# Performance work log

Measured on AMD Instinct MI355X. Metric: run time of the kernel, lower is better.

The kernel has to match this reference:

```python
import jax, jax.numpy as jnp
import numpy as np

B, L, DIM, H = 1, 2048, 3072, 24
D = DIM // H  # 128
EPS = 1e-6

def setup_inputs() -> dict:
    key = jax.random.key(0)
    ks = jax.random.split(key, 7)
    x = jax.random.normal(ks[0], (B, L, DIM), dtype=jnp.float32)
    pe = jax.random.normal(ks[1], (B, 1, L, D // 2, 2, 2), dtype=jnp.float32)
    w_qkv = jax.random.normal(ks[2], (DIM, 3 * DIM), dtype=jnp.float32) / np.sqrt(DIM)
    q_scale = jnp.ones((D,), dtype=jnp.float32)
    k_scale = jnp.ones((D,), dtype=jnp.float32)
    w_proj = jax.random.normal(ks[3], (DIM, DIM), dtype=jnp.float32) / np.sqrt(DIM)
    b_proj = jnp.zeros((DIM,), dtype=jnp.float32)
    return {"x": x, "pe": pe, "w_qkv": w_qkv, "q_scale": q_scale,
            "k_scale": k_scale, "w_proj": w_proj, "b_proj": b_proj}

def _rmsnorm(t, scale):
    # flax nn.RMSNorm: t * rsqrt(mean(t^2, -1) + eps) * scale
    ms = jnp.mean(jnp.square(t), axis=-1, keepdims=True)
    return t * jax.lax.rsqrt(ms + EPS) * scale

def _apply_rope(xq, xk, pe):
    # xq/xk: [B,H,L,D]; pe: [B,1,L,D/2,2,2]
    xq_ = xq.reshape(*xq.shape[:-1], -1, 1, 2)
    xk_ = xk.reshape(*xk.shape[:-1], -1, 1, 2)
    xq_out = pe[..., 0] * xq_[..., 0] + pe[..., 1] * xq_[..., 1]
    xk_out = pe[..., 0] * xk_[..., 0] + pe[..., 1] * xk_[..., 1]
    return xq_out.reshape(xq.shape), xk_out.reshape(xk.shape)

def reference(x, pe, w_qkv, q_scale, k_scale, w_proj, b_proj):
    qkv = jnp.einsum('bld,de->ble', x, w_qkv)            # [B,L,3*DIM]
    qkv = qkv.reshape(B, L, 3, H, D)
    qkv = jnp.moveaxis(qkv, 2, 0)                          # [3,B,H?,..]
    q, k, v = jnp.transpose(qkv, (0, 1, 3, 2, 4))          # each [B,H,L,D]
    q = _rmsnorm(q, q_scale).astype(v.dtype)
    k = _rmsnorm(k, k_scale).astype(v.dtype)
    q, k = _apply_rope(q, k, pe)
    scale = 1.0 / np.sqrt(D)
    scores = jnp.einsum('bhqd,bhkd->bhqk', q, k) * scale   # [B,H,L,L]
    attn = jax.nn.softmax(scores, axis=-1)
    out = jnp.einsum('bhqk,bhkd->bhqd', attn, v)           # [B,H,L,D]
    out = jnp.transpose(out, (0, 2, 1, 3)).reshape(B, L, DIM)
    return jnp.einsum('bld,de->ble', out, w_proj) + b_proj
```

## Files before the change

### kernel.cpp

```cpp
#include <hip/hip_runtime.h>

#define L_    2048
#define DIM_  3072
#define H_    24
#define D_    128
#define NQKV  9216

typedef __attribute__((ext_vector_type(8))) short bf16x8;
typedef __attribute__((ext_vector_type(4))) short bf16x4;
typedef __attribute__((ext_vector_type(4))) float f32x4;

__device__ __forceinline__ unsigned short f2bf(float f) {
  union { float f; unsigned u; } v; v.f = f;
  unsigned r = v.u + 0x7fffu + ((v.u >> 16) & 1u);
  return (unsigned short)(r >> 16);
}
__device__ __forceinline__ float bf2f(unsigned short h) {
  union { unsigned u; float f; } v; v.u = ((unsigned)h) << 16;
  return v.f;
}

__device__ __forceinline__ void gload_lds16(const void* g, void* l) {
  auto* lp = reinterpret_cast<__attribute__((address_space(3))) unsigned int*>(
      reinterpret_cast<uintptr_t>(l));
  auto* gp = reinterpret_cast<const __attribute__((address_space(1))) unsigned int*>(
      reinterpret_cast<uintptr_t>(g));
  __builtin_amdgcn_global_load_lds(gp, lp, 16, 0, 0);
}

__global__ void cast_f32_to_bf16(const float* __restrict__ in,
                                 unsigned short* __restrict__ out, int n) {
  int total = n >> 2;
  int stride = gridDim.x * blockDim.x;
  for (int i = blockIdx.x * blockDim.x + threadIdx.x; i < total; i += stride) {
    float4 v = ((const float4*)in)[i];
    ushort4 o;
    o.x = f2bf(v.x); o.y = f2bf(v.y); o.z = f2bf(v.z); o.w = f2bf(v.w);
    ((ushort4*)out)[i] = o;
  }
}

__global__ __launch_bounds__(256)
void castT_f32_bf16(const float* __restrict__ in, unsigned short* __restrict__ out,
                    int K, int N) {
  int k = blockIdx.x * 256 + threadIdx.x;
  int n0 = blockIdx.y * 128;
  const float* src = in + (size_t)k * N;
  #pragma unroll 8
  for (int j = 0; j < 128; j++)
    out[(size_t)(n0 + j) * K + k] = f2bf(src[n0 + j]);
}

template<bool OUT_BF16, bool BIAS>
__global__ __launch_bounds__(256, 3)
void gemm_bt(const unsigned short* __restrict__ A,
             const unsigned short* __restrict__ Bt,
             void* __restrict__ Cout, const float* __restrict__ bias,
             int M, int N, int K)
{
  __shared__ unsigned short As[128 * 64];
  __shared__ unsigned short Bs[128 * 64];
  const int tid  = threadIdx.x;
  const int wave = tid >> 6;
  const int lane = tid & 63;
  const int l15  = lane & 15;
  const int quad = lane >> 4;
  const int wm = wave >> 1, wn = wave & 1;
  const int bm = blockIdx.y * 128;
  const int bn = blockIdx.x * 128;

  const int srow = lane >> 3;
  const int scol = (lane & 7) ^ srow;
  const unsigned short* Ag = A  + (size_t)(bm + wave * 32 + srow) * K + scol * 8;
  const unsigned short* Bg = Bt + (size_t)(bn + wave * 32 + srow) * K + scol * 8;
  unsigned short* Al = &As[(wave * 32) * 64];
  unsigned short* Bl = &Bs[(wave * 32) * 64];

  f32x4 acc[4][4];
  #pragma unroll
  for (int i = 0; i < 4; i++)
    #pragma unroll
    for (int j = 0; j < 4; j++) acc[i][j] = (f32x4){0.f, 0.f, 0.f, 0.f};

  for (int k0 = 0; k0 < K; k0 += 64) {
    __syncthreads();
    #pragma unroll
    for (int j = 0; j < 4; j++) {
      gload_lds16(Ag + (size_t)j * 8 * K + k0, Al + j * 8 * 64);
      gload_lds16(Bg + (size_t)j * 8 * K + k0, Bl + j * 8 * 64);
    }
    __syncthreads();
    #pragma unroll
    for (int ks = 0; ks < 2; ks++) {
      const int cph = ((ks * 4 + quad) ^ (l15 & 7)) * 8;
      bf16x8 af[4], bf[4];
      #pragma unroll
      for (int mt = 0; mt < 4; mt++)
        af[mt] = *(const bf16x8*)&As[(wm * 64 + mt * 16 + l15) * 64 + cph];
      #pragma unroll
      for (int nt = 0; nt < 4; nt++)
        bf[nt] = *(const bf16x8*)&Bs[(wn * 64 + nt * 16 + l15) * 64 + cph];
      #pragma unroll
      for (int mt = 0; mt < 4; mt++)
        #pragma unroll
        for (int nt = 0; nt < 4; nt++)
          acc[mt][nt] = __builtin_amdgcn_mfma_f32_16x16x32_bf16(
              af[mt], bf[nt], acc[mt][nt], 0, 0, 0);
    }
  }
  #pragma unroll
  for (int mt = 0; mt < 4; mt++)
    #pragma unroll
    for (int nt = 0; nt < 4; nt++)
      #pragma unroll
      for (int r = 0; r < 4; r++) {
        int row = bm + wm * 64 + mt * 16 + quad * 4 + r;
        int col = bn + wn * 64 + nt * 16 + l15;
        float v = acc[mt][nt][r];
        if (BIAS) v += bias[col];
        if (OUT_BF16)
          ((unsigned short*)Cout)[(size_t)row * N + col] = f2bf(v);
        else
          ((float*)Cout)[(size_t)row * N + col] = v;
      }
}

__global__ __launch_bounds__(128)
void qkv_post(const unsigned short* __restrict__ qkv,
              const float* __restrict__ pe,
              const float* __restrict__ q_scale,
              const float* __restrict__ k_scale,
              unsigned short* __restrict__ Qo,
              unsigned short* __restrict__ Ko)
{
  const int l = blockIdx.x;
  const int h = blockIdx.y;
  const int d = threadIdx.x;
  const int wave = d >> 6;
  const unsigned short* row = qkv + (size_t)l * NQKV + h * D_;
  float qv = bf2f(row[d]);
  float kv = bf2f(row[DIM_ + d]);
  float q2 = qv * qv, k2 = kv * kv;
  #pragma unroll
  for (int mask = 1; mask < 64; mask <<= 1) {
    q2 += __shfl_xor(q2, mask);
    k2 += __shfl_xor(k2, mask);
  }
  __shared__ float sq[2], sk[2];
  __shared__ float qbuf[128], kbuf[128];
  if ((d & 63) == 0) { sq[wave] = q2; sk[wave] = k2; }
  __syncthreads();
  float msq = (sq[0] + sq[1]) * (1.f / 128.f);
  float msk = (sk[0] + sk[1]) * (1.f / 128.f);
  qbuf[d] = qv * rsqrtf(msq + 1e-6f) * q_scale[d];
  kbuf[d] = kv * rsqrtf(msk + 1e-6f) * k_scale[d];
  __syncthreads();
  int p = d >> 1, s = d & 1;
  const float* pel = pe + (((size_t)l * 64 + p) * 2 + s) * 2;
  float a = pel[0], b = pel[1];
  float qr = (a * qbuf[2 * p] + b * qbuf[2 * p + 1]) * 0.08838834764831845f;
  float kr =  a * kbuf[2 * p] + b * kbuf[2 * p + 1];
  size_t o = ((size_t)h * L_ + l) * D_ + d;
  Qo[o] = f2bf(qr);
  Ko[o] = f2bf(kr);
}

__global__ __launch_bounds__(256)
void v_transpose(const unsigned short* __restrict__ qkv,
                 unsigned short* __restrict__ Vt) {
  int h = blockIdx.y;
  int l = blockIdx.x * 256 + threadIdx.x;
  const unsigned short* src = qkv + (size_t)l * NQKV + 2 * DIM_ + h * D_;
  unsigned short* dst = Vt + (size_t)h * D_ * L_ + l;
  #pragma unroll
  for (int c = 0; c < 16; c++) {
    uint4 v = *(const uint4*)&src[c * 8];
    const unsigned short* pv = (const unsigned short*)&v;
    #pragma unroll
    for (int j = 0; j < 8; j++)
      dst[(size_t)(c * 8 + j) * L_] = pv[j];
  }
}

__global__ __launch_bounds__(256, 3)
void flash_attn(const unsigned short* __restrict__ Q,
                const unsigned short* __restrict__ K,
                const unsigned short* __restrict__ Vt,
                unsigned short* __restrict__ Out)
{
  __shared__ __align__(16) char smem[34304];
  unsigned short* Ks = (unsigned short*)smem;
  unsigned short* Vs = Ks + 8192;
  float*  Obuf = (float*)smem;
  float2* mlb  = (float2*)(smem + 32768);
  float4* sAr  = (float4*)(smem + 33280);

  const int tid  = threadIdx.x;
  const int wave = tid >> 6;
  const int lane = tid & 63;
  const int l15  = lane & 15;
  const int quad = lane >> 4;
  const int qg = wave >> 1;
  const int kh = wave & 1;
  const int h  = blockIdx.y;
  const int q0 = blockIdx.x * 64 + qg * 32;

  const unsigned short* Qh = Q  + (size_t)h * L_ * D_;
  const unsigned short* Kh = K  + (size_t)h * L_ * D_;
  const unsigned short* Vh = Vt + (size_t)h * D_ * L_;

  bf16x8 qf[2][4];
  #pragma unroll
  for (int nt = 0; nt < 2; nt++)
    #pragma unroll
    for (int kc = 0; kc < 4; kc++)
      qf[nt][kc] = *(const bf16x8*)&Qh[(size_t)(q0 + nt * 16 + l15) * D_ + kc * 32 + quad * 8];

  f32x4 oacc[2][8];
  #pragma unroll
  for (int i = 0; i < 2; i++)
    #pragma unroll
    for (int j = 0; j < 8; j++) oacc[i][j] = (f32x4){0.f, 0.f, 0.f, 0.f};
  float m_i[2] = {-1e30f, -1e30f}, l_i[2] = {0.f, 0.f};

  const int kr_l = lane >> 4;
  const int vr_l = lane >> 3;
  const int vcl  = (lane & 7) ^ vr_l;

  for (int t = 0; t < L_; t += 64) {
    __syncthreads();
    #pragma unroll
    for (int ji = 0; ji < 4; ji++) {
      int Rr = wave * 16 + ji * 4;
      int cl = (lane & 15) ^ ((Rr + kr_l) & 15);
      gload_lds16(&Kh[(size_t)(t + Rr + kr_l) * D_ + cl * 8], &Ks[Rr * 128]);
      int R2 = wave * 32 + ji * 8;
      gload_lds16(&Vh[(size_t)(R2 + vr_l) * L_ + t + vcl * 8], &Vs[R2 * 64]);
    }
    __syncthreads();

    f32x4 s[2][2];
    #pragma unroll
    for (int i = 0; i < 2; i++)
      #pragma unroll
      for (int j = 0; j < 2; j++) s[i][j] = (f32x4){0.f, 0.f, 0.f, 0.f};
    #pragma unroll
    for (int mt = 0; mt < 2; mt++) {
      const int krow = kh * 32 + mt * 16 + l15;
      #pragma unroll
      for (int kc = 0; kc < 4; kc++) {
        bf16x8 kf = *(const bf16x8*)&Ks[krow * 128 + (((kc * 4 + quad) ^ l15) * 8)];
        s[mt][0] = __builtin_amdgcn_mfma_f32_16x16x32_bf16(kf, qf[0][kc], s[mt][0], 0, 0, 0);
        s[mt][1] = __builtin_amdgcn_mfma_f32_16x16x32_bf16(kf, qf[1][kc], s[mt][1], 0, 0, 0);
      }
    }
    float vmax[2], alpha[2], rs[2];
    #pragma unroll
    for (int nt = 0; nt < 2; nt++) {
      vmax[nt] = fmaxf(fmaxf(fmaxf(s[0][nt][0], s[0][nt][1]), fmaxf(s[0][nt][2], s[0][nt][3])),
                       fmaxf(fmaxf(s[1][nt][0], s[1][nt][1]), fmaxf(s[1][nt][2], s[1][nt][3])));
      vmax[nt] = fmaxf(vmax[nt], __shfl_xor(vmax[nt], 16));
      vmax[nt] = fmaxf(vmax[nt], __shfl_xor(vmax[nt], 32));
      float mnew = fmaxf(m_i[nt], vmax[nt]);
      alpha[nt] = __expf(m_i[nt] - mnew);
      m_i[nt] = mnew;
      rs[nt] = 0.f;
    }
    #pragma unroll
    for (int mt = 0; mt < 2; mt++)
      #pragma unroll
      for (int nt = 0; nt < 2; nt++)
        #pragma unroll
        for (int r = 0; r < 4; r++) {
          float p = __expf(s[mt][nt][r] - m_i[nt]);
          s[mt][nt][r] = p;
          rs[nt] += p;
        }
    #pragma unroll
    for (int nt = 0; nt < 2; nt++) {
      rs[nt] += __shfl_xor(rs[nt], 16);
      rs[nt] += __shfl_xor(rs[nt], 32);
      l_i[nt] = l_i[nt] * alpha[nt] + rs[nt];
    }
    float ar[2][4];
    #pragma unroll
    for (int qt = 0; qt < 2; qt++)
      #pragma unroll
      for (int r = 0; r < 4; r++)
        ar[qt][r] = __shfl(alpha[qt], quad * 4 + r);
    #pragma unroll
    for (int qt = 0; qt < 2; qt++)
      #pragma unroll
      for (int ntd = 0; ntd < 8; ntd++)
        #pragma unroll
        for (int r = 0; r < 4; r++)
          oacc[qt][ntd][r] *= ar[qt][r];
    bf16x4 pk[2][2];
    #pragma unroll
    for (int mt = 0; mt < 2; mt++)
      #pragma unroll
      for (int qt = 0; qt < 2; qt++)
        pk[mt][qt] = (bf16x4){(short)f2bf(s[mt][qt][0]), (short)f2bf(s[mt][qt][1]),
                              (short)f2bf(s[mt][qt][2]), (short)f2bf(s[mt][qt][3])};
    #pragma unroll
    for (int ntd = 0; ntd < 8; ntd++) {
      const int vrow = ntd * 16 + l15;
      #pragma unroll
      for (int mt = 0; mt < 2; mt++) {
        int phys = (kh * 4 + mt * 2 + (quad >> 1)) ^ (l15 & 7);
        bf16x4 vf = *(const bf16x4*)&Vs[vrow * 64 + phys * 8 + (quad & 1) * 4];
        oacc[0][ntd] = __builtin_amdgcn_mfma_f32_16x16x16bf16_1k(pk[mt][0], vf, oacc[0][ntd], 0, 0, 0);
        oacc[1][ntd] = __builtin_amdgcn_mfma_f32_16x16x16bf16_1k(pk[mt][1], vf, oacc[1][ntd], 0, 0, 0);
      }
    }
  }

  __syncthreads();
  if (kh == 1) {
    #pragma unroll
    for (int qt = 0; qt < 2; qt++)
      #pragma unroll
      for (int ntd = 0; ntd < 8; ntd++)
        #pragma unroll
        for (int r = 0; r < 4; r++)
          Obuf[(size_t)(qg * 32 + qt * 16 + quad * 4 + r) * 128 + ntd * 16 + l15] = oacc[qt][ntd][r];
    if (quad == 0)
      #pragma unroll
      for (int qt = 0; qt < 2; qt++)
        mlb[qg * 32 + qt * 16 + l15] = make_float2(m_i[qt], l_i[qt]);
  }
  __syncthreads();
  if (kh == 0 && quad == 0) {
    #pragma unroll
    for (int qt = 0; qt < 2; qt++) {
      float2 m1 = mlb[qg * 32 + qt * 16 + l15];
      float M  = fmaxf(m_i[qt], m1.x);
      float a0 = __expf(m_i[qt] - M);
      float a1 = __expf(m1.x - M);
      float Ls = l_i[qt] * a0 + m1.y * a1;
      sAr[qg * 32 + qt * 16 + l15] = make_float4(a0, a1, 1.f / Ls, 0.f);
    }
  }
  __syncthreads();
  if (kh == 0) {
    #pragma unroll
    for (int qt = 0; qt < 2; qt++)
      #pragma unroll
      for (int r = 0; r < 4; r++) {
        float4 A = sAr[qg * 32 + qt * 16 + quad * 4 + r];
        #pragma unroll
        for (int ntd = 0; ntd < 8; ntd++) {
          float o1 = Obuf[(size_t)(qg * 32 + qt * 16 + quad * 4 + r) * 128 + ntd * 16 + l15];
          float v  = (oacc[qt][ntd][r] * A.x + o1 * A.y) * A.z;
          Out[(size_t)(q0 + qt * 16 + quad * 4 + r) * DIM_ + h * D_ + ntd * 16 + l15] = f2bf(v);
        }
      }
  }
}

extern "C" void kernel_launch(void* const* d_in, const int* in_sizes, int n_in,
                              void* d_out, int out_size, void* d_ws, size_t ws_size,
                              hipStream_t stream) {
  const float* x       = (const float*)d_in[0];
  const float* pe      = (const float*)d_in[1];
  const float* w_qkv   = (const float*)d_in[2];
  const float* q_scale = (const float*)d_in[3];
  const float* k_scale = (const float*)d_in[4];
  const float* w_proj  = (const float*)d_in[5];
  const float* b_proj  = (const float*)d_in[6];

  unsigned short* w_qkvT  = (unsigned short*)d_ws;
  unsigned short* w_projT = w_qkvT + 28311552;
  unsigned short* x_b     = w_projT + 9437184;
  unsigned short* qkv_b   = x_b + 6291456;
  unsigned short* q_r     = qkv_b + 18874368;
  unsigned short* k_r     = q_r + 6291456;
  unsigned short* vt_r    = k_r + 6291456;
  unsigned short* attn_b  = qkv_b;

  cast_f32_to_bf16<<<2048, 256, 0, stream>>>(x, x_b, 6291456);
  castT_f32_bf16<<<dim3(12, 72), 256, 0, stream>>>(w_qkv, w_qkvT, 3072, 9216);
  castT_f32_bf16<<<dim3(12, 24), 256, 0, stream>>>(w_proj, w_projT, 3072, 3072);

  gemm_bt<true, false><<<dim3(72, 16), 256, 0, stream>>>(
      x_b, w_qkvT, qkv_b, nullptr, 2048, 9216, 3072);

  qkv_post<<<dim3(2048, 24), 128, 0, stream>>>(
      qkv_b, pe, q_scale, k_scale, q_r, k_r);
  v_transpose<<<dim3(8, 24), 256, 0, stream>>>(qkv_b, vt_r);

  flash_attn<<<dim3(32, 24), 256, 0, stream>>>(q_r, k_r, vt_r, attn_b);

  gemm_bt<false, true><<<dim3(24, 16), 256, 0, stream>>>(
      attn_b, w_projT, d_out, b_proj, 2048, 3072, 3072);
}
```

Baseline: 559.5 us.

## Fuse RMSNorm and RoPE into QKV GEMM epilogue, vectorize weight transpose-cast

Adds a dedicated QKV GEMM whose epilogue does per-head RMSNorm (cross-wave row reduction through LDS), RoPE and Q scaling in fp32 registers, writing Q/K directly in head-major layout and V to a separate buffer. This removes the qkv_post kernel and the round trip of the full QKV tensor through global memory in bf16, and avoids one bf16 rounding before normalization. The weight transpose-cast now reads float4 per row. The epilogue adds shuffles, an extra sync and scattered pe loads to the GEMM tail.

```diff
diff --git a/kernel.cpp b/kernel.cpp
--- a/kernel.cpp
+++ b/kernel.cpp
@@ -14,10 +14,6 @@
   union { float f; unsigned u; } v; v.f = f;
   unsigned r = v.u + 0x7fffu + ((v.u >> 16) & 1u);
   return (unsigned short)(r >> 16);
-}
-__device__ __forceinline__ float bf2f(unsigned short h) {
-  union { unsigned u; float f; } v; v.u = ((unsigned)h) << 16;
-  return v.f;
 }
 
 __device__ __forceinline__ void gload_lds16(const void* g, void* l) {
@@ -45,10 +41,133 @@
                     int K, int N) {
   int k = blockIdx.x * 256 + threadIdx.x;
   int n0 = blockIdx.y * 128;
-  const float* src = in + (size_t)k * N;
-  #pragma unroll 8
-  for (int j = 0; j < 128; j++)
-    out[(size_t)(n0 + j) * K + k] = f2bf(src[n0 + j]);
+  const float* src = in + (size_t)k * N + n0;
+  #pragma unroll 4
+  for (int j4 = 0; j4 < 32; j4++) {
+    float4 v = *(const float4*)&src[j4 * 4];
+    out[(size_t)(n0 + j4 * 4 + 0) * K + k] = f2bf(v.x);
+    out[(size_t)(n0 + j4 * 4 + 1) * K + k] = f2bf(v.y);
+    out[(size_t)(n0 + j4 * 4 + 2) * K + k] = f2bf(v.z);
+    out[(size_t)(n0 + j4 * 4 + 3) * K + k] = f2bf(v.w);
+  }
+}
+
+__global__ __launch_bounds__(256, 3)
+void gemm_qkv(const unsigned short* __restrict__ A,
+              const unsigned short* __restrict__ Bt,
+              const float* __restrict__ pe,
+              const float* __restrict__ q_scale,
+              const float* __restrict__ k_scale,
+              unsigned short* __restrict__ Qo,
+              unsigned short* __restrict__ Ko,
+              unsigned short* __restrict__ Vo)
+{
+  const int M = L_, N = NQKV, K = DIM_;
+  __shared__ unsigned short As[128 * 64];
+  __shared__ unsigned short Bs[128 * 64];
+  const int tid  = threadIdx.x;
+  const int wave = tid >> 6;
+  const int lane = tid & 63;
+  const int l15  = lane & 15;
+  const int quad = lane >> 4;
+  const int wm = wave >> 1, wn = wave & 1;
+  const int bm = blockIdx.y * 128;
+  const int bn = blockIdx.x * 128;
+
+  const int srow = lane >> 3;
+  const int scol = (lane & 7) ^ srow;
+  const unsigned short* Ag = A  + (size_t)(bm + wave * 32 + srow) * K + scol * 8;
+  const unsigned short* Bg = Bt + (size_t)(bn + wave * 32 + srow) * K + scol * 8;
+  unsigned short* Al = &As[(wave * 32) * 64];
+  unsigned short* Bl = &Bs[(wave * 32) * 64];
+
+  f32x4 acc[4][4];
+  #pragma unroll
+  for (int i = 0; i < 4; i++)
+    #pragma unroll
+    for (int j = 0; j < 4; j++) acc[i][j] = (f32x4){0.f, 0.f, 0.f, 0.f};
+
+  for (int k0 = 0; k0 < K; k0 += 64) {
+    __syncthreads();
+    #pragma unroll
+    for (int j = 0; j < 4; j++) {
+      gload_lds16(Ag + (size_t)j * 8 * K + k0, Al + j * 8 * 64);
+      gload_lds16(Bg + (size_t)j * 8 * K + k0, Bl + j * 8 * 64);
+    }
+    __syncthreads();
+    #pragma unroll
+    for (int ks = 0; ks < 2; ks++) {
+      const int cph = ((ks * 4 + quad) ^ (l15 & 7)) * 8;
+      bf16x8 af[4], bf[4];
+      #pragma unroll
+      for (int mt = 0; mt < 4; mt++)
+        af[mt] = *(const bf16x8*)&As[(wm * 64 + mt * 16 + l15) * 64 + cph];
+      #pragma unroll
+      for (int nt = 0; nt < 4; nt++)
+        bf[nt] = *(const bf16x8*)&Bs[(wn * 64 + nt * 16 + l15) * 64 + cph];
+      #pragma unroll
+      for (int mt = 0; mt < 4; mt++)
+        #pragma unroll
+        for (int nt = 0; nt < 4; nt++)
+          acc[mt][nt] = __builtin_amdgcn_mfma_f32_16x16x32_bf16(
+              af[mt], bf[nt], acc[mt][nt], 0, 0, 0);
+    }
+  }
+  __syncthreads();
+
+  const int bnx = blockIdx.x;
+  if (bnx < 48) {
+    const bool isQ = bnx < 24;
+    const int  hh  = isQ ? bnx : bnx - 24;
+    const float* sc = isQ ? q_scale : k_scale;
+    unsigned short* dst = isQ ? Qo : Ko;
+    float* rbuf = (float*)As;
+    #pragma unroll
+    for (int mt = 0; mt < 4; mt++)
+      #pragma unroll
+      for (int r = 0; r < 4; r++) {
+        float p = 0.f;
+        #pragma unroll
+        for (int nt = 0; nt < 4; nt++) p += acc[mt][nt][r] * acc[mt][nt][r];
+        p += __shfl_xor(p, 1); p += __shfl_xor(p, 2);
+        p += __shfl_xor(p, 4); p += __shfl_xor(p, 8);
+        if (l15 == 0) rbuf[wn * 128 + wm * 64 + mt * 16 + quad * 4 + r] = p;
+      }
+    __syncthreads();
+    #pragma unroll
+    for (int mt = 0; mt < 4; mt++)
+      #pragma unroll
+      for (int r = 0; r < 4; r++) {
+        const int lrow = wm * 64 + mt * 16 + quad * 4 + r;
+        const int lg = bm + lrow;
+        float ms = (rbuf[lrow] + rbuf[128 + lrow]) * (1.f / 128.f);
+        float rinv = rsqrtf(ms + 1e-6f);
+        #pragma unroll
+        for (int nt = 0; nt < 4; nt++) {
+          const int d = wn * 64 + nt * 16 + l15;
+          float n  = acc[mt][nt][r] * rinv * sc[d];
+          float np = __shfl_xor(n, 1);
+          float2 ab = *(const float2*)&pe[(size_t)lg * 256 + (d >> 1) * 4 + (d & 1) * 2];
+          float xe = (d & 1) ? np : n;
+          float xo = (d & 1) ? n  : np;
+          float o = ab.x * xe + ab.y * xo;
+          if (isQ) o *= 0.08838834764831845f;
+          dst[((size_t)hh * L_ + lg) * D_ + d] = f2bf(o);
+        }
+      }
+  } else {
+    const int hh = bnx - 48;
+    #pragma unroll
+    for (int mt = 0; mt < 4; mt++)
+      #pragma unroll
+      for (int nt = 0; nt < 4; nt++)
+        #pragma unroll
+        for (int r = 0; r < 4; r++) {
+          int row = bm + wm * 64 + mt * 16 + quad * 4 + r;
+          int col = hh * D_ + wn * 64 + nt * 16 + l15;
+          Vo[(size_t)row * DIM_ + col] = f2bf(acc[mt][nt][r]);
+        }
+  }
 }
 
 template<bool OUT_BF16, bool BIAS>
@@ -125,52 +244,12 @@
       }
 }
 
-__global__ __launch_bounds__(128)
-void qkv_post(const unsigned short* __restrict__ qkv,
-              const float* __restrict__ pe,
-              const float* __restrict__ q_scale,
-              const float* __restrict__ k_scale,
-              unsigned short* __restrict__ Qo,
-              unsigned short* __restrict__ Ko)
-{
-  const int l = blockIdx.x;
-  const int h = blockIdx.y;
-  const int d = threadIdx.x;
-  const int wave = d >> 6;
-  const unsigned short* row = qkv + (size_t)l * NQKV + h * D_;
-  float qv = bf2f(row[d]);
-  float kv = bf2f(row[DIM_ + d]);
-  float q2 = qv * qv, k2 = kv * kv;
-  #pragma unroll
-  for (int mask = 1; mask < 64; mask <<= 1) {
-    q2 += __shfl_xor(q2, mask);
-    k2 += __shfl_xor(k2, mask);
-  }
-  __shared__ float sq[2], sk[2];
-  __shared__ float qbuf[128], kbuf[128];
-  if ((d & 63) == 0) { sq[wave] = q2; sk[wave] = k2; }
-  __syncthreads();
-  float msq = (sq[0] + sq[1]) * (1.f / 128.f);
-  float msk = (sk[0] + sk[1]) * (1.f / 128.f);
-  qbuf[d] = qv * rsqrtf(msq + 1e-6f) * q_scale[d];
-  kbuf[d] = kv * rsqrtf(msk + 1e-6f) * k_scale[d];
-  __syncthreads();
-  int p = d >> 1, s = d & 1;
-  const float* pel = pe + (((size_t)l * 64 + p) * 2 + s) * 2;
-  float a = pel[0], b = pel[1];
-  float qr = (a * qbuf[2 * p] + b * qbuf[2 * p + 1]) * 0.08838834764831845f;
-  float kr =  a * kbuf[2 * p] + b * kbuf[2 * p + 1];
-  size_t o = ((size_t)h * L_ + l) * D_ + d;
-  Qo[o] = f2bf(qr);
-  Ko[o] = f2bf(kr);
-}
-
 __global__ __launch_bounds__(256)
-void v_transpose(const unsigned short* __restrict__ qkv,
+void v_transpose(const unsigned short* __restrict__ v_buf,
                  unsigned short* __restrict__ Vt) {
   int h = blockIdx.y;
   int l = blockIdx.x * 256 + threadIdx.x;
-  const unsigned short* src = qkv + (size_t)l * NQKV + 2 * DIM_ + h * D_;
+  const unsigned short* src = v_buf + (size_t)l * DIM_ + h * D_;
   unsigned short* dst = Vt + (size_t)h * D_ * L_ + l;
   #pragma unroll
   for (int c = 0; c < 16; c++) {
@@ -372,22 +451,20 @@
   unsigned short* w_qkvT  = (unsigned short*)d_ws;
   unsigned short* w_projT = w_qkvT + 28311552;
   unsigned short* x_b     = w_projT + 9437184;
-  unsigned short* qkv_b   = x_b + 6291456;
-  unsigned short* q_r     = qkv_b + 18874368;
+  unsigned short* v_buf   = x_b + 6291456;
+  unsigned short* q_r     = v_buf + 6291456;
   unsigned short* k_r     = q_r + 6291456;
   unsigned short* vt_r    = k_r + 6291456;
-  unsigned short* attn_b  = qkv_b;
+  unsigned short* attn_b  = vt_r + 6291456;
 
   cast_f32_to_bf16<<<2048, 256, 0, stream>>>(x, x_b, 6291456);
   castT_f32_bf16<<<dim3(12, 72), 256, 0, stream>>>(w_qkv, w_qkvT, 3072, 9216);
   castT_f32_bf16<<<dim3(12, 24), 256, 0, stream>>>(w_proj, w_projT, 3072, 3072);
 
-  gemm_bt<true, false><<<dim3(72, 16), 256, 0, stream>>>(
-      x_b, w_qkvT, qkv_b, nullptr, 2048, 9216, 3072);
-
-  qkv_post<<<dim3(2048, 24), 128, 0, stream>>>(
-      qkv_b, pe, q_scale, k_scale, q_r, k_r);
-  v_transpose<<<dim3(8, 24), 256, 0, stream>>>(qkv_b, vt_r);
+  gemm_qkv<<<dim3(72, 16), 256, 0, stream>>>(
+      x_b, w_qkvT, pe, q_scale, k_scale, q_r, k_r, v_buf);
+
+  v_transpose<<<dim3(8, 24), 256, 0, stream>>>(v_buf, vt_r);
 
   flash_attn<<<dim3(32, 24), 256, 0, stream>>>(q_r, k_r, vt_r, attn_b);
 
```

After: 569.1 us. Within noise of the previous version (+1.7%).
